# Optimization experiments

Measured on AMD Instinct MI355X. Metric: run time of the kernel, lower is better.

Reference implementation:

```python
import jax, jax.numpy as jnp
import numpy as np

PAD = 0  # module-level global in the original repo (MT convention)


def setup_inputs() -> dict:
    key = jax.random.key(0)
    k1, k2, k3 = jax.random.split(key, 3)
    N, V, D = 2048, 32000, 512
    # realistic log-probabilities over the vocab
    pred_ll = jax.nn.log_softmax(jax.random.normal(k1, (N, V), jnp.float32), axis=-1)
    target = jax.random.randint(k2, (N,), 0, V)
    # frozen pretrained word-vector table (nn.Embedding.from_pretrained)
    emb = jax.random.normal(k3, (V, D), jnp.float32)
    return {"pred_ll": pred_ll, "target": target, "emb": emb}


def reference(pred_ll, target, emb):
    # pred_ll: [N, V] log-probs; target: [N] int ids; emb: [V, D] frozen table
    mask = (target != PAD).astype(pred_ll.dtype)  # [N] non-pad mask

    # nll_loss = -pred_ll.gather(-1, target) summed over non-pad tokens
    nll = -jnp.take_along_axis(pred_ll, target[:, None], axis=-1)[:, 0]  # [N]
    nll_loss = jnp.sum(nll * mask)

    # pairwise L2 distance gold-embedding vs full table, via the GEMM identity
    # ||g - e||^2 = ||g||^2 + ||e||^2 - 2 g.e  (avoids the [N, V, D] tensor)
    g = emb[target]                                    # [N, D]
    g2 = jnp.sum(g * g, axis=-1, keepdims=True)        # [N, 1]
    e2 = jnp.sum(emb * emb, axis=-1)[None, :]          # [1, V]
    d2 = jnp.maximum(g2 + e2 - 2.0 * (g @ emb.T), 0.0)  # [N, V]
    dist = jnp.sqrt(jnp.maximum(d2, 1e-12))             # [N, V], L2 distances

    dist_max = jnp.max(dist, axis=1, keepdims=True)    # [N, 1]
    w = jax.nn.softmax(dist_max - jnp.abs(dist), axis=1)  # [N, V]

    # loss = sum_v softmax_weight * (-log p), summed over non-pad tokens
    loss = jnp.sum(w * (-pred_ll), axis=1)             # [N]
    return (jnp.sum(loss * mask), nll_loss)
```

## Files before the change

kernel.cpp:

```cpp
#include <hip/hip_runtime.h>
#include <float.h>

#define NTOK   2048
#define VOCAB  32000
#define DIM    512
#define NCHUNK 64
#define NT32   (VOCAB / 32)
#define ROWSB  128
#define NRB    (NTOK / ROWSB)
#define TILE_BYTES 16384

typedef __attribute__((ext_vector_type(4))) float f32x4;
typedef unsigned int u32;
typedef long long i64;

__device__ __forceinline__ i64 pack_fp8x8(f32x4 x0, f32x4 x1) {
    int lo = __builtin_amdgcn_cvt_pk_fp8_f32(x0.x, x0.y, 0, false);
    lo = __builtin_amdgcn_cvt_pk_fp8_f32(x0.z, x0.w, lo, true);
    int hi = __builtin_amdgcn_cvt_pk_fp8_f32(x1.x, x1.y, 0, false);
    hi = __builtin_amdgcn_cvt_pk_fp8_f32(x1.z, x1.w, hi, true);
    return (i64)(((unsigned long long)(u32)hi << 32) | (u32)lo);
}

__device__ __forceinline__ void async_copy16(void* lds, const void* g) {
    __builtin_amdgcn_global_load_lds(
        (const __attribute__((address_space(1))) u32*)(const u32*)g,
        (__attribute__((address_space(3))) u32*)(u32*)lds, 16, 0, 0);
}

__global__ void init_out(float* out) {
    if (threadIdx.x < 2) out[threadIdx.x] = 0.f;
}

__global__ __launch_bounds__(256) void precast_kernel(
    const float* __restrict__ emb, char* __restrict__ Bbf, float* __restrict__ e2) {
    const int tile = blockIdx.x;
    const int t = threadIdx.x, w = t >> 6, l = t & 63;
    const int v0 = tile * 32;
    char* tbase = Bbf + (size_t)tile * TILE_BYTES;
    #pragma unroll
    for (int it = 0; it < 8; ++it) {
        const int v = it * 4 + w;
        const float* src = emb + (size_t)(v0 + v) * DIM + l * 8;
        f32x4 x0 = *(const f32x4*)src;
        f32x4 x1 = *(const f32x4*)(src + 4);
        float sq = x0.x*x0.x + x0.y*x0.y + x0.z*x0.z + x0.w*x0.w
                 + x1.x*x1.x + x1.y*x1.y + x1.z*x1.z + x1.w*x1.w;
        #pragma unroll
        for (int m = 1; m < 64; m <<= 1) sq += __shfl_xor(sq, m);
        if (l == 0) e2[v0 + v] = sq;
        *(i64*)(tbase + (l >> 2) * 1024 + (v >> 4) * 512
                + (((l & 3) * 16 + (v & 15)) * 8)) = pack_fp8x8(x0, x1);
    }
}

__global__ __launch_bounds__(256) void e2_kernel(const float* __restrict__ emb,
                                                 float* __restrict__ e2) {
    int gid = blockIdx.x * 256 + threadIdx.x;
    int wid = gid >> 6, l = gid & 63;
    if (wid >= VOCAB) return;
    const float* row = emb + (size_t)wid * DIM + l * 8;
    f32x4 a = *(const f32x4*)row;
    f32x4 b = *(const f32x4*)(row + 4);
    float s = a.x*a.x + a.y*a.y + a.z*a.z + a.w*a.w
            + b.x*b.x + b.y*b.y + b.z*b.z + b.w*b.w;
    #pragma unroll
    for (int m = 1; m < 64; m <<= 1) s += __shfl_xor(s, m);
    if (l == 0) e2[wid] = s;
}

template<bool PRECAST>
__global__ __launch_bounds__(256, 3) void fused_kernel(
    const float* __restrict__ pred_ll, const int* __restrict__ target,
    const float* __restrict__ emb, const char* __restrict__ Bbf,
    const float* __restrict__ e2g,
    float* __restrict__ partials ) {

    const int rb = blockIdx.x;
    const int ch = blockIdx.y;
    const int t  = threadIdx.x;
    const int w  = t >> 6;
    const int l  = t & 63;
    const int l15 = l & 15;
    const int lg  = l >> 4;

    __shared__ char ldsB[2][TILE_BYTES];

    const int t0 = (ch * NT32) >> 6;
    const int t1 = ((ch + 1) * NT32) >> 6;
    const int rowbase = rb * ROWSB + w * 32;

    i64 afrag[2][16];
    #pragma unroll
    for (int rs = 0; rs < 2; ++rs) {
        const int grow = target[rowbase + rs * 16 + l15];
        if constexpr (PRECAST) {
            const char* ab = Bbf + (size_t)(grow >> 5) * TILE_BYTES
                           + ((grow & 31) >> 4) * 512
                           + ((l & 48) + (grow & 15)) * 8;
            #pragma unroll
            for (int ks = 0; ks < 16; ++ks)
                afrag[rs][ks] = *(const i64*)(ab + ks * 1024);
        } else {
            const float* gsrc = emb + (size_t)grow * DIM;
            #pragma unroll
            for (int ks = 0; ks < 16; ++ks) {
                const int k0 = ks * 32 + ((l >> 4) << 3);
                afrag[rs][ks] = pack_fp8x8(*(const f32x4*)(gsrc + k0),
                                           *(const f32x4*)(gsrc + k0 + 4));
            }
        }
    }
    float g2[2][4];
    #pragma unroll
    for (int rs = 0; rs < 2; ++rs)
        #pragma unroll
        for (int r = 0; r < 4; ++r)
            g2[rs][r] = e2g[target[rowbase + rs * 16 + lg * 4 + r]];

    float s_[2][4] = {{0,0,0,0},{0,0,0,0}};
    float ac_[2][4] = {{0,0,0,0},{0,0,0,0}};

    auto stage = [&](int buf, int tg) {
        if constexpr (PRECAST) {
            const char* src = Bbf + (size_t)tg * TILE_BYTES;
            #pragma unroll
            for (int it = 0; it < 4; ++it)
                async_copy16(ldsB[buf] + it * 4096 + t * 16, src + it * 4096 + t * 16);
        } else {
            const int v0 = tg * 32;
            #pragma unroll
            for (int it = 0; it < 8; ++it) {
                const int slot = it * 256 + t;
                const int ks = slot >> 7, c = (slot >> 6) & 1, il = slot & 63;
                const int v = c * 16 + (il & 15);
                const int k0 = ks * 32 + ((il >> 4) << 3);
                const float* src = emb + (size_t)(v0 + v) * DIM + k0;
                *(i64*)(ldsB[buf] + ks * 1024 + c * 512 + il * 8) =
                    pack_fp8x8(*(const f32x4*)src, *(const f32x4*)(src + 4));
            }
        }
    };

    stage(0, t0);

    int cur = 0;
    #pragma unroll 1
    for (int tg = t0; tg < t1; ++tg) {
        if (tg + 1 < t1) {
            stage(cur ^ 1, tg + 1);
            if constexpr (PRECAST)
                asm volatile("s_waitcnt vmcnt(4)" ::: "memory");
            else
                asm volatile("s_waitcnt vmcnt(0) lgkmcnt(0)" ::: "memory");
        } else {
            asm volatile("s_waitcnt vmcnt(0) lgkmcnt(0)" ::: "memory");
        }
        __builtin_amdgcn_s_barrier();

        const int v0 = tg * 32;
        float e2v[2], q[2][2][4];
        #pragma unroll
        for (int cs = 0; cs < 2; ++cs) {
            e2v[cs] = e2g[v0 + cs * 16 + l15];
            const size_t p0 = (size_t)rowbase * VOCAB + v0 + cs * 16 + l15;
            #pragma unroll
            for (int rs = 0; rs < 2; ++rs)
                #pragma unroll
                for (int r = 0; r < 4; ++r)
                    q[cs][rs][r] = pred_ll[p0 + (size_t)(rs * 16 + lg * 4 + r) * VOCAB];
        }

        f32x4 acc[2][2] = {{{0,0,0,0},{0,0,0,0}},{{0,0,0,0},{0,0,0,0}}};
        const char* lb = ldsB[cur];
        #pragma unroll
        for (int ks = 0; ks < 16; ++ks) {
            const i64 b0 = *(const i64*)(lb + ks * 1024 + l * 8);
            const i64 b1 = *(const i64*)(lb + ks * 1024 + 512 + l * 8);
            acc[0][0] = __builtin_amdgcn_mfma_f32_16x16x32_fp8_fp8(afrag[0][ks], b0, acc[0][0], 0, 0, 0);
            acc[1][0] = __builtin_amdgcn_mfma_f32_16x16x32_fp8_fp8(afrag[1][ks], b0, acc[1][0], 0, 0, 0);
            acc[0][1] = __builtin_amdgcn_mfma_f32_16x16x32_fp8_fp8(afrag[0][ks], b1, acc[0][1], 0, 0, 0);
            acc[1][1] = __builtin_amdgcn_mfma_f32_16x16x32_fp8_fp8(afrag[1][ks], b1, acc[1][1], 0, 0, 0);
        }

        #pragma unroll
        for (int cs = 0; cs < 2; ++cs)
            #pragma unroll
            for (int rs = 0; rs < 2; ++rs)
                #pragma unroll
                for (int r = 0; r < 4; ++r) {
                    float d2 = fmaxf(fmaf(-2.f, acc[rs][cs][r], g2[rs][r] + e2v[cs]), 1e-12f);
                    const float e = __expf(-sqrtf(d2));
                    s_[rs][r] += e;
                    ac_[rs][r] = fmaf(e, -q[cs][rs][r], ac_[rs][r]);
                }

        asm volatile("" ::: "memory");
        __builtin_amdgcn_s_barrier();
        cur ^= 1;
    }

    #pragma unroll
    for (int rs = 0; rs < 2; ++rs)
        #pragma unroll
        for (int r = 0; r < 4; ++r) {
            float sv = s_[rs][r], av = ac_[rs][r];
            #pragma unroll
            for (int m = 1; m < 16; m <<= 1) {
                sv += __shfl_xor(sv, m);
                av += __shfl_xor(av, m);
            }
            if (l15 == 0) {
                const int rg = rowbase + rs * 16 + lg * 4 + r;
                float* pp = partials + ((size_t)rg * NCHUNK + ch) * 2;
                pp[0] = sv; pp[1] = av;
            }
        }
}

__global__ __launch_bounds__(256) void reduce_kernel(
    const float* __restrict__ pred_ll, const int* __restrict__ target,
    const float* __restrict__ partials, float* __restrict__ out) {
    const int row = blockIdx.x * 256 + threadIdx.x;
    float loss = 0.f, nll = 0.f;
    if (row < NTOK) {
        const int tg = target[row];
        const float mask = (tg != 0) ? 1.f : 0.f;
        const float* pp = partials + (size_t)row * NCHUNK * 2;
        float S = 0.f, A = 0.f;
        #pragma unroll 8
        for (int c = 0; c < NCHUNK; ++c) { S += pp[c * 2]; A += pp[c * 2 + 1]; }
        loss = mask * (A / S);
        nll  = mask * (-pred_ll[(size_t)row * VOCAB + tg]);
    }
    #pragma unroll
    for (int o = 32; o > 0; o >>= 1) {
        loss += __shfl_xor(loss, o);
        nll  += __shfl_xor(nll, o);
    }
    if ((threadIdx.x & 63) == 0) {
        atomicAdd(&out[0], loss);
        atomicAdd(&out[1], nll);
    }
}

extern "C" void kernel_launch(void* const* d_in, const int* in_sizes, int n_in,
                              void* d_out, int out_size, void* d_ws, size_t ws_size,
                              hipStream_t stream) {
    const float* pred_ll = (const float*)d_in[0];
    const int*   target  = (const int*)d_in[1];
    const float* emb     = (const float*)d_in[2];
    float* out = (float*)d_out;

    float* e2       = (float*)d_ws;
    float* partials = e2 + VOCAB;
    const size_t base = (size_t)VOCAB * 4 + (size_t)NTOK * NCHUNK * 2 * 4;
    char* Bbf       = (char*)d_ws + base;
    const size_t need = base + (size_t)NT32 * TILE_BYTES;
    const bool precast = (ws_size >= need);

    hipLaunchKernelGGL(init_out, dim3(1), dim3(64), 0, stream, out);
    if (precast) {
        hipLaunchKernelGGL(precast_kernel, dim3(NT32), dim3(256), 0, stream, emb, Bbf, e2);
        hipLaunchKernelGGL((fused_kernel<true>), dim3(NRB, NCHUNK), dim3(256), 0, stream,
                           pred_ll, target, emb, Bbf, e2, partials);
    } else {
        hipLaunchKernelGGL(e2_kernel, dim3(VOCAB * 64 / 256), dim3(256), 0, stream, emb, e2);
        hipLaunchKernelGGL((fused_kernel<false>), dim3(NRB, NCHUNK), dim3(256), 0, stream,
                           pred_ll, target, emb, Bbf, e2, partials);
    }
    hipLaunchKernelGGL(reduce_kernel, dim3(NTOK / 256), dim3(256), 0, stream,
                       pred_ll, target, partials, out);
}
```

Baseline: 157.5 us.

## Triple-buffer LDS tiles and prefetch pred_ll one tile ahead, single barrier

Replaces the double-buffered LDS tile loop with a three-slot ring that stages the B tile two iterations ahead. The pred_ll and e2 values for the next tile are loaded into registers one iteration early. The trailing barrier is removed, leaving one barrier per iteration with a vmcnt wait sized for the outstanding loads. The chunk count also changes from 64 to 50 so each chunk gets an equal number of tiles. This costs more LDS (48KB per block, which may limit occupancy at 3 blocks/CU) and more registers, and the hard-coded vmcnt(22) must match the actual number of in-flight loads.

```diff
diff --git a/kernel.cpp b/kernel.cpp
--- a/kernel.cpp
+++ b/kernel.cpp
@@ -4,8 +4,9 @@
 #define NTOK   2048
 #define VOCAB  32000
 #define DIM    512
-#define NCHUNK 64
+#define NCHUNK 50
 #define NT32   (VOCAB / 32)
+#define TPC    (NT32 / NCHUNK)
 #define ROWSB  128
 #define NRB    (NTOK / ROWSB)
 #define TILE_BYTES 16384
@@ -84,10 +85,9 @@
     const int l15 = l & 15;
     const int lg  = l >> 4;
 
-    __shared__ char ldsB[2][TILE_BYTES];
-
-    const int t0 = (ch * NT32) >> 6;
-    const int t1 = ((ch + 1) * NT32) >> 6;
+    __shared__ char ldsB[3][TILE_BYTES];
+
+    const int t0 = ch * TPC, t1 = t0 + TPC;
     const int rowbase = rb * ROWSB + w * 32;
 
     i64 afrag[2][16];
@@ -121,7 +121,7 @@
     float s_[2][4] = {{0,0,0,0},{0,0,0,0}};
     float ac_[2][4] = {{0,0,0,0},{0,0,0,0}};
 
-    auto stage = [&](int buf, int tg) {
+    auto stageF = [&](int buf, int tg) {
         if constexpr (PRECAST) {
             const char* src = Bbf + (size_t)tg * TILE_BYTES;
             #pragma unroll
@@ -141,38 +141,56 @@
             }
         }
     };
-
-    stage(0, t0);
-
-    int cur = 0;
-    #pragma unroll 1
-    for (int tg = t0; tg < t1; ++tg) {
-        if (tg + 1 < t1) {
-            stage(cur ^ 1, tg + 1);
-            if constexpr (PRECAST)
-                asm volatile("s_waitcnt vmcnt(4)" ::: "memory");
-            else
-                asm volatile("s_waitcnt vmcnt(0) lgkmcnt(0)" ::: "memory");
-        } else {
-            asm volatile("s_waitcnt vmcnt(0) lgkmcnt(0)" ::: "memory");
-        }
-        __builtin_amdgcn_s_barrier();
-
+    auto loadQ = [&](int tg, float (&qq)[2][2][4]) {
         const int v0 = tg * 32;
-        float e2v[2], q[2][2][4];
         #pragma unroll
         for (int cs = 0; cs < 2; ++cs) {
-            e2v[cs] = e2g[v0 + cs * 16 + l15];
             const size_t p0 = (size_t)rowbase * VOCAB + v0 + cs * 16 + l15;
             #pragma unroll
             for (int rs = 0; rs < 2; ++rs)
                 #pragma unroll
                 for (int r = 0; r < 4; ++r)
-                    q[cs][rs][r] = pred_ll[p0 + (size_t)(rs * 16 + lg * 4 + r) * VOCAB];
+                    qq[cs][rs][r] = pred_ll[p0 + (size_t)(rs * 16 + lg * 4 + r) * VOCAB];
+        }
+    };
+
+    float qA[2][2][4], qB[2][2][4];
+    float e2A[2], e2B[2];
+
+    stageF(0, t0);
+    asm volatile("" ::: "memory");
+    stageF(1, t0 + 1);
+    asm volatile("" ::: "memory");
+    loadQ(t0, qB);
+    { const int v0 = t0 * 32; e2B[0] = e2g[v0 + l15]; e2B[1] = e2g[v0 + 16 + l15]; }
+
+    int ibr = 0;
+    #pragma unroll 1
+    for (int tg = t0; tg < t1; ++tg) {
+        asm volatile("s_waitcnt vmcnt(22)" ::: "memory");
+        if constexpr (!PRECAST) asm volatile("s_waitcnt lgkmcnt(0)" ::: "memory");
+        __builtin_amdgcn_s_barrier();
+
+        #pragma unroll
+        for (int cs = 0; cs < 2; ++cs) {
+            e2A[cs] = e2B[cs];
+            #pragma unroll
+            for (int rs = 0; rs < 2; ++rs)
+                #pragma unroll
+                for (int r = 0; r < 4; ++r) qA[cs][rs][r] = qB[cs][rs][r];
+        }
+
+        const int ibw = (ibr >= 1) ? ibr - 1 : ibr + 2;
+        if (tg + 2 < t1) stageF(ibw, tg + 2);
+        if (tg + 1 < t1) {
+            loadQ(tg + 1, qB);
+            const int v0n = (tg + 1) * 32;
+            e2B[0] = e2g[v0n + l15];
+            e2B[1] = e2g[v0n + 16 + l15];
         }
 
         f32x4 acc[2][2] = {{{0,0,0,0},{0,0,0,0}},{{0,0,0,0},{0,0,0,0}}};
-        const char* lb = ldsB[cur];
+        const char* lb = ldsB[ibr];
         #pragma unroll
         for (int ks = 0; ks < 16; ++ks) {
             const i64 b0 = *(const i64*)(lb + ks * 1024 + l * 8);
@@ -189,15 +207,13 @@
             for (int rs = 0; rs < 2; ++rs)
                 #pragma unroll
                 for (int r = 0; r < 4; ++r) {
-                    float d2 = fmaxf(fmaf(-2.f, acc[rs][cs][r], g2[rs][r] + e2v[cs]), 1e-12f);
+                    float d2 = fmaxf(fmaf(-2.f, acc[rs][cs][r], g2[rs][r] + e2A[cs]), 1e-12f);
                     const float e = __expf(-sqrtf(d2));
                     s_[rs][r] += e;
-                    ac_[rs][r] = fmaf(e, -q[cs][rs][r], ac_[rs][r]);
+                    ac_[rs][r] = fmaf(e, -qA[cs][rs][r], ac_[rs][r]);
                 }
 
-        asm volatile("" ::: "memory");
-        __builtin_amdgcn_s_barrier();
-        cur ^= 1;
+        ibr = (ibr >= 2) ? 0 : ibr + 1;
     }
 
     #pragma unroll
@@ -228,7 +244,7 @@
         const float mask = (tg != 0) ? 1.f : 0.f;
         const float* pp = partials + (size_t)row * NCHUNK * 2;
         float S = 0.f, A = 0.f;
-        #pragma unroll 8
+        #pragma unroll 5
         for (int c = 0; c < NCHUNK; ++c) { S += pp[c * 2]; A += pp[c * 2 + 1]; }
         loss = mask * (A / S);
         nll  = mask * (-pred_ll[(size_t)row * VOCAB + tg]);
```

After: 182.2 us. 15.7% more time.
